# Optimization experiments

Measured on AMD Instinct MI355X. Metric: run time of the kernel, lower is better.

The kernel has to match this reference:

```python
import jax, jax.numpy as jnp
import numpy as np

N_NODES = 100000


def gcn_conv(x, edge_index, W, b, n_nodes):
    # h = X W  (transform first, aggregate in the smaller hidden dim)
    h = x @ W
    src, dst = edge_index[0], edge_index[1]
    # add self-loops (GCNConv default, fill_value=1)
    loop = jnp.arange(n_nodes, dtype=src.dtype)
    src = jnp.concatenate([src, loop])
    dst = jnp.concatenate([dst, loop])
    w = jnp.ones(src.shape[0], dtype=x.dtype)
    # symmetric degree normalization: deg^{-1/2}[src] * w * deg^{-1/2}[dst]
    deg = jax.ops.segment_sum(w, dst, num_segments=n_nodes)
    dinv = jnp.where(deg > 0, jax.lax.rsqrt(deg), 0.0).astype(x.dtype)
    norm = dinv[src] * w * dinv[dst]
    # gather messages from src, scale, scatter-add into dst
    out = jax.ops.segment_sum(h[src] * norm[:, None], dst, num_segments=n_nodes)
    return out + b


def setup_inputs() -> dict:
    key = jax.random.key(0)
    k1, k2, k3, k4 = jax.random.split(key, 4)
    n, f, hid, c, e = N_NODES, 512, 64, 40, 1600000
    x = jax.random.normal(k1, (n, f), dtype=jnp.float32)
    edge_index = jax.random.randint(k2, (2, e), 0, n, dtype=jnp.int64)
    W1 = jax.random.normal(k3, (f, hid), dtype=jnp.float32) * (1.0 / np.sqrt(f))
    b1 = jnp.zeros((hid,), dtype=jnp.float32)
    W2 = jax.random.normal(k4, (hid, c), dtype=jnp.float32) * (1.0 / np.sqrt(hid))
    b2 = jnp.zeros((c,), dtype=jnp.float32)
    return {"x": x, "edge_index": edge_index, "W1": W1, "b1": b1, "W2": W2, "b2": b2}


def reference(x, edge_index, W1, b1, W2, b2):
    h = jax.nn.relu(gcn_conv(x, edge_index, W1, b1, N_NODES))
    # dropout is identity at inference (training=False)
    h = gcn_conv(h, edge_index, W2, b2, N_NODES)
    return jax.nn.log_softmax(h, axis=1)
```

## Files before the change

kernel.cpp:

```cpp
#include <hip/hip_runtime.h>
#include <hip/hip_bf16.h>
#include <hip/hip_fp16.h>
#include <cstddef>

#define N_NODES 100000
#define F_IN    512
#define HID     64
#define NCLS    40

#define CAP       64
#define CUR_PAD   16

#define NPART       8
#define PART_NODES  12500
#define PART_BLOCKS 256

using half8 = __attribute__((ext_vector_type(8))) _Float16;
using f32x4 = __attribute__((ext_vector_type(4))) float;

__global__ void zero_kernel(int* __restrict__ p, int n) {
    int i = blockIdx.x * blockDim.x + threadIdx.x;
    if (i < n) p[i] = 0;
}

__global__ __launch_bounds__(256) void scatter_part_kernel(const int* __restrict__ src,
                                                           const int* __restrict__ dst,
                                                           int* __restrict__ cur,
                                                           int* __restrict__ ebuf, int E) {
    const int p  = blockIdx.x & (NPART - 1);
    const int bi = blockIdx.x >> 3;
    const int nb = gridDim.x >> 3;
    const int lo = p * PART_NODES, hi = lo + PART_NODES;
    for (int e = bi * 256 + (int)threadIdx.x; e < E; e += nb * 256) {
        int d = dst[e];
        if (d >= lo && d < hi) {
            int pos = atomicAdd(&cur[d * CUR_PAD], 1);
            if (pos < CAP) ebuf[(size_t)d * CAP + pos] = src[e];
        }
    }
}

__global__ void make_dinv_kernel(const int* __restrict__ cur, float* __restrict__ dinv, int n) {
    int i = blockIdx.x * blockDim.x + threadIdx.x;
    if (i < n) dinv[i] = rsqrtf((float)(cur[i * CUR_PAD] + 1));
}

__global__ __launch_bounds__(256) void gemm1_mfma_kernel(const float* __restrict__ X,
                                                         const float* __restrict__ W,
                                                         __half* __restrict__ H, int M) {
    __shared__ _Float16 As[4][64][8];
    __shared__ _Float16 Bs[4][64][8];

    const int tid  = threadIdx.x;
    const int lane = tid & 63;
    const int w    = tid >> 6;
    const int l15  = lane & 15;
    const int kg   = lane >> 4;
    const int rowBase = blockIdx.x * 64;

    f32x4 acc[4] = {};

    for (int kt = 0; kt < F_IN; kt += 32) {
        #pragma unroll
        for (int p = 0; p < 2; ++p) {
            int idx = tid * 2 + p;
            int r = idx >> 3, k4 = idx & 7;
            int gr = rowBase + r; if (gr >= M) gr = M - 1;
            const float4 v = *reinterpret_cast<const float4*>(
                &X[(size_t)gr * F_IN + kt + k4 * 4]);
            _Float16* dstp = &As[k4 >> 1][r][(k4 & 1) * 4];
            dstp[0] = (_Float16)v.x; dstp[1] = (_Float16)v.y;
            dstp[2] = (_Float16)v.z; dstp[3] = (_Float16)v.w;
        }
        #pragma unroll
        for (int p = 0; p < 2; ++p) {
            int idx = tid * 2 + p;
            int k = idx >> 4, c4 = idx & 15;
            const float4 v = *reinterpret_cast<const float4*>(
                &W[(size_t)(kt + k) * HID + c4 * 4]);
            int kgg = k >> 3, j = k & 7;
            Bs[kgg][c4 * 4 + 0][j] = (_Float16)v.x;
            Bs[kgg][c4 * 4 + 1][j] = (_Float16)v.y;
            Bs[kgg][c4 * 4 + 2][j] = (_Float16)v.z;
            Bs[kgg][c4 * 4 + 3][j] = (_Float16)v.w;
        }
        __syncthreads();

        const half8 a = *reinterpret_cast<const half8*>(&As[kg][w * 16 + l15][0]);
        #pragma unroll
        for (int ct = 0; ct < 4; ++ct) {
            const half8 b = *reinterpret_cast<const half8*>(&Bs[kg][ct * 16 + l15][0]);
            acc[ct] = __builtin_amdgcn_mfma_f32_16x16x32_f16(a, b, acc[ct], 0, 0, 0);
        }
        __syncthreads();
    }

    #pragma unroll
    for (int ct = 0; ct < 4; ++ct) {
        #pragma unroll
        for (int r = 0; r < 4; ++r) {
            int grow = rowBase + w * 16 + kg * 4 + r;
            if (grow < M) H[(size_t)grow * HID + ct * 16 + l15] = __float2half(acc[ct][r]);
        }
    }
}

__global__ __launch_bounds__(256) void agg1_kernel(const __half* __restrict__ h,
                                                   const int* __restrict__ ebuf,
                                                   const int* __restrict__ cur,
                                                   const float* __restrict__ dinv,
                                                   const float* __restrict__ b1,
                                                   __half* __restrict__ z, int M) {
    const int lane = threadIdx.x & 63;
    const int n = blockIdx.x * 4 + (threadIdx.x >> 6);
    if (n >= M) return;

    const float di = dinv[n];
    float acc = __half2float(h[(size_t)n * HID + lane]) * di * di;

    const int cnt = min(cur[n * CUR_PAD], CAP);
    const int* win = &ebuf[(size_t)n * CAP];

    int   s  = 0;
    float nm = 0.f;
    if (lane < cnt) {
        s  = win[lane];
        nm = dinv[s] * di;
    }
    int j = 0;
    for (; j + 4 <= cnt; j += 4) {
        int sa = __shfl(s, j);
        int sb = __shfl(s, j + 1);
        int sc = __shfl(s, j + 2);
        int sd = __shfl(s, j + 3);
        float na = __shfl(nm, j);
        float nb = __shfl(nm, j + 1);
        float nc = __shfl(nm, j + 2);
        float nd = __shfl(nm, j + 3);
        float va = __half2float(h[(size_t)sa * HID + lane]);
        float vb = __half2float(h[(size_t)sb * HID + lane]);
        float vc = __half2float(h[(size_t)sc * HID + lane]);
        float vd = __half2float(h[(size_t)sd * HID + lane]);
        acc = fmaf(va, na, acc);
        acc = fmaf(vb, nb, acc);
        acc = fmaf(vc, nc, acc);
        acc = fmaf(vd, nd, acc);
    }
    for (; j < cnt; ++j) {
        int sj = __shfl(s, j);
        float nj = __shfl(nm, j);
        acc = fmaf(__half2float(h[(size_t)sj * HID + lane]), nj, acc);
    }

    acc = fmaxf(acc + b1[lane], 0.0f);
    z[(size_t)n * HID + lane] = __float2half(acc);
}

__global__ __launch_bounds__(256) void gemm2_kernel(const __half* __restrict__ z,
                                                    const float* __restrict__ W2,
                                                    __half* __restrict__ h2, int M) {
    __shared__ float W2s[HID * NCLS];
    __shared__ float zs[64 * HID];

    const int tid = threadIdx.x;
    const int rowBase = blockIdx.x * 64;

    for (int i = tid; i < HID * NCLS; i += 256) W2s[i] = W2[i];

    #pragma unroll
    for (int p = 0; p < 2; ++p) {
        int o = tid * 2 + p;
        int r = o >> 3, c8 = o & 7;
        int gr = rowBase + r;
        float4 raw = make_float4(0.f, 0.f, 0.f, 0.f);
        if (gr < M) raw = *reinterpret_cast<const float4*>(&z[(size_t)gr * HID + c8 * 8]);
        const __half2* hp = reinterpret_cast<const __half2*>(&raw);
        #pragma unroll
        for (int q = 0; q < 4; ++q) {
            float2 f = __half22float2(hp[q]);
            zs[r * HID + c8 * 8 + q * 2]     = f.x;
            zs[r * HID + c8 * 8 + q * 2 + 1] = f.y;
        }
    }
    __syncthreads();

    #pragma unroll
    for (int p = 0; p < 10; ++p) {
        int o = p * 256 + tid;
        int r = o / NCLS, j = o - r * NCLS;
        float s = 0.f;
        #pragma unroll
        for (int k = 0; k < HID; ++k) s = fmaf(zs[r * HID + k], W2s[k * NCLS + j], s);
        int gr = rowBase + r;
        if (gr < M) h2[(size_t)gr * 64 + j] = __float2half(s);
    }
}

__global__ __launch_bounds__(256) void agg2_lsm_kernel(const __half* __restrict__ h2,
                                                       const int* __restrict__ ebuf,
                                                       const int* __restrict__ cur,
                                                       const float* __restrict__ dinv,
                                                       const float* __restrict__ b2,
                                                       float* __restrict__ out, int M) {
    const int lane = threadIdx.x & 63;
    const int n = blockIdx.x * 4 + (threadIdx.x >> 6);
    if (n >= M) return;

    const bool act = (lane < NCLS);
    const float di = dinv[n];
    float acc = act ? __half2float(h2[(size_t)n * 64 + lane]) * di * di : 0.f;

    const int cnt = min(cur[n * CUR_PAD], CAP);
    const int* win = &ebuf[(size_t)n * CAP];

    int   s  = 0;
    float nm = 0.f;
    if (lane < cnt) {
        s  = win[lane];
        nm = dinv[s] * di;
    }
    int j = 0;
    for (; j + 4 <= cnt; j += 4) {
        int sa = __shfl(s, j);
        int sb = __shfl(s, j + 1);
        int sc = __shfl(s, j + 2);
        int sd = __shfl(s, j + 3);
        float na = __shfl(nm, j);
        float nb = __shfl(nm, j + 1);
        float nc = __shfl(nm, j + 2);
        float nd = __shfl(nm, j + 3);
        if (act) {
            float va = __half2float(h2[(size_t)sa * 64 + lane]);
            float vb = __half2float(h2[(size_t)sb * 64 + lane]);
            float vc = __half2float(h2[(size_t)sc * 64 + lane]);
            float vd = __half2float(h2[(size_t)sd * 64 + lane]);
            acc = fmaf(va, na, acc);
            acc = fmaf(vb, nb, acc);
            acc = fmaf(vc, nc, acc);
            acc = fmaf(vd, nd, acc);
        }
    }
    for (; j < cnt; ++j) {
        int sj = __shfl(s, j);
        float nj = __shfl(nm, j);
        if (act) acc = fmaf(__half2float(h2[(size_t)sj * 64 + lane]), nj, acc);
    }

    float logit = act ? (acc + b2[lane]) : -1e30f;
    float m = logit;
    #pragma unroll
    for (int o = 32; o >= 1; o >>= 1) m = fmaxf(m, __shfl_xor(m, o));
    float ex = act ? __expf(logit - m) : 0.f;
    float sm = ex;
    #pragma unroll
    for (int o = 32; o >= 1; o >>= 1) sm += __shfl_xor(sm, o);
    float res = logit - m - __logf(sm);

    if (act) out[(size_t)n * NCLS + lane] = res;
}

extern "C" void kernel_launch(void* const* d_in, const int* in_sizes, int n_in,
                              void* d_out, int out_size, void* d_ws, size_t ws_size,
                              hipStream_t stream) {
    const float* x  = (const float*)d_in[0];
    const int*   ei = (const int*)d_in[1];
    const float* W1 = (const float*)d_in[2];
    const float* b1 = (const float*)d_in[3];
    const float* W2 = (const float*)d_in[4];
    const float* b2 = (const float*)d_in[5];
    float* out = (float*)d_out;

    const int M = N_NODES;
    const int E = in_sizes[1] / 2;
    const int* src = ei;
    const int* dst = ei + E;

    char* ws = (char*)d_ws;
    int*    cur  = (int*)   (ws + 0);
    float*  dinv = (float*) (ws + 6400000);
    int*    ebuf = (int*)   (ws + 6800000);
    __half* h1   = (__half*)(ws + 32400000);
    __half* z    = (__half*)(ws + 45200000);
    __half* h2   = (__half*)(ws + 58000000);

    zero_kernel<<<(M * CUR_PAD + 255) / 256, 256, 0, stream>>>(cur, M * CUR_PAD);

    scatter_part_kernel<<<NPART * PART_BLOCKS, 256, 0, stream>>>(src, dst, cur, ebuf, E);
    make_dinv_kernel<<<(M + 255) / 256, 256, 0, stream>>>(cur, dinv, M);

    gemm1_mfma_kernel<<<(M + 63) / 64, 256, 0, stream>>>(x, W1, h1, M);

    agg1_kernel<<<(M + 3) / 4, 256, 0, stream>>>(h1, ebuf, cur, dinv, b1, z, M);

    gemm2_kernel<<<(M + 63) / 64, 256, 0, stream>>>(z, W2, h2, M);
    agg2_lsm_kernel<<<(M + 3) / 4, 256, 0, stream>>>(h2, ebuf, cur, dinv, b2, out, M);
}
```

Before: 295.5 us.

## Fuse layer-1 aggregation with second GEMM and unpad degree counters

Merges the layer-1 aggregation kernel with the 64x40 second transform, so each block aggregates four nodes, keeps the ReLU outputs in shared memory and multiplies them by W2 directly. This removes the z intermediate buffer, one kernel launch, and the global-memory round trip for z. It also drops the 16-int padding on the per-node atomic counters, which shrinks the zeroing and counter traffic but may bring back contention from atomics that share a cache line. In exchange, every block reloads the whole W2 into shared memory and only 160 of 256 threads take part in the small GEMM.

```diff
diff --git a/kernel.cpp b/kernel.cpp
--- a/kernel.cpp
+++ b/kernel.cpp
@@ -9,7 +9,6 @@
 #define NCLS    40
 
 #define CAP       64
-#define CUR_PAD   16
 
 #define NPART       8
 #define PART_NODES  12500
@@ -34,7 +33,7 @@
     for (int e = bi * 256 + (int)threadIdx.x; e < E; e += nb * 256) {
         int d = dst[e];
         if (d >= lo && d < hi) {
-            int pos = atomicAdd(&cur[d * CUR_PAD], 1);
+            int pos = atomicAdd(&cur[d], 1);
             if (pos < CAP) ebuf[(size_t)d * CAP + pos] = src[e];
         }
     }
@@ -42,7 +41,7 @@
 
 __global__ void make_dinv_kernel(const int* __restrict__ cur, float* __restrict__ dinv, int n) {
     int i = blockIdx.x * blockDim.x + threadIdx.x;
-    if (i < n) dinv[i] = rsqrtf((float)(cur[i * CUR_PAD] + 1));
+    if (i < n) dinv[i] = rsqrtf((float)(cur[i] + 1));
 }
 
 __global__ __launch_bounds__(256) void gemm1_mfma_kernel(const float* __restrict__ X,
@@ -105,20 +104,27 @@
     }
 }
 
-__global__ __launch_bounds__(256) void agg1_kernel(const __half* __restrict__ h,
-                                                   const int* __restrict__ ebuf,
-                                                   const int* __restrict__ cur,
-                                                   const float* __restrict__ dinv,
-                                                   const float* __restrict__ b1,
-                                                   __half* __restrict__ z, int M) {
-    const int lane = threadIdx.x & 63;
-    const int n = blockIdx.x * 4 + (threadIdx.x >> 6);
-    if (n >= M) return;
+__global__ __launch_bounds__(256) void agg1_gemm2_kernel(const __half* __restrict__ h,
+                                                         const int* __restrict__ ebuf,
+                                                         const int* __restrict__ cur,
+                                                         const float* __restrict__ dinv,
+                                                         const float* __restrict__ b1,
+                                                         const float* __restrict__ W2,
+                                                         __half* __restrict__ h2) {
+    __shared__ float W2s[HID * NCLS];
+    __shared__ float zt[4][HID];
+
+    const int tid  = threadIdx.x;
+    const int lane = tid & 63;
+    const int wv   = tid >> 6;
+    const int n    = blockIdx.x * 4 + wv;
+
+    for (int i = tid; i < HID * NCLS; i += 256) W2s[i] = W2[i];
 
     const float di = dinv[n];
     float acc = __half2float(h[(size_t)n * HID + lane]) * di * di;
 
-    const int cnt = min(cur[n * CUR_PAD], CAP);
+    const int cnt = min(cur[n], CAP);
     const int* win = &ebuf[(size_t)n * CAP];
 
     int   s  = 0;
@@ -152,47 +158,16 @@
         acc = fmaf(__half2float(h[(size_t)sj * HID + lane]), nj, acc);
     }
 
-    acc = fmaxf(acc + b1[lane], 0.0f);
-    z[(size_t)n * HID + lane] = __float2half(acc);
-}
-
-__global__ __launch_bounds__(256) void gemm2_kernel(const __half* __restrict__ z,
-                                                    const float* __restrict__ W2,
-                                                    __half* __restrict__ h2, int M) {
-    __shared__ float W2s[HID * NCLS];
-    __shared__ float zs[64 * HID];
-
-    const int tid = threadIdx.x;
-    const int rowBase = blockIdx.x * 64;
-
-    for (int i = tid; i < HID * NCLS; i += 256) W2s[i] = W2[i];
-
-    #pragma unroll
-    for (int p = 0; p < 2; ++p) {
-        int o = tid * 2 + p;
-        int r = o >> 3, c8 = o & 7;
-        int gr = rowBase + r;
-        float4 raw = make_float4(0.f, 0.f, 0.f, 0.f);
-        if (gr < M) raw = *reinterpret_cast<const float4*>(&z[(size_t)gr * HID + c8 * 8]);
-        const __half2* hp = reinterpret_cast<const __half2*>(&raw);
-        #pragma unroll
-        for (int q = 0; q < 4; ++q) {
-            float2 f = __half22float2(hp[q]);
-            zs[r * HID + c8 * 8 + q * 2]     = f.x;
-            zs[r * HID + c8 * 8 + q * 2 + 1] = f.y;
-        }
-    }
+    zt[wv][lane] = fmaxf(acc + b1[lane], 0.0f);
     __syncthreads();
 
-    #pragma unroll
-    for (int p = 0; p < 10; ++p) {
-        int o = p * 256 + tid;
-        int r = o / NCLS, j = o - r * NCLS;
-        float s = 0.f;
-        #pragma unroll
-        for (int k = 0; k < HID; ++k) s = fmaf(zs[r * HID + k], W2s[k * NCLS + j], s);
-        int gr = rowBase + r;
-        if (gr < M) h2[(size_t)gr * 64 + j] = __float2half(s);
+    if (tid < 4 * NCLS) {
+        int r = tid / NCLS, c = tid - r * NCLS;
+        float sacc = 0.f;
+        #pragma unroll
+        for (int k = 0; k < HID; ++k)
+            sacc = fmaf(zt[r][k], W2s[k * NCLS + c], sacc);
+        h2[(size_t)(blockIdx.x * 4 + r) * 64 + c] = __float2half(sacc);
     }
 }
 
@@ -210,7 +185,7 @@
     const float di = dinv[n];
     float acc = act ? __half2float(h2[(size_t)n * 64 + lane]) * di * di : 0.f;
 
-    const int cnt = min(cur[n * CUR_PAD], CAP);
+    const int cnt = min(cur[n], CAP);
     const int* win = &ebuf[(size_t)n * CAP];
 
     int   s  = 0;
@@ -277,21 +252,19 @@
 
     char* ws = (char*)d_ws;
     int*    cur  = (int*)   (ws + 0);
-    float*  dinv = (float*) (ws + 6400000);
-    int*    ebuf = (int*)   (ws + 6800000);
-    __half* h1   = (__half*)(ws + 32400000);
-    __half* z    = (__half*)(ws + 45200000);
-    __half* h2   = (__half*)(ws + 58000000);
-
-    zero_kernel<<<(M * CUR_PAD + 255) / 256, 256, 0, stream>>>(cur, M * CUR_PAD);
+    float*  dinv = (float*) (ws + 409600);
+    int*    ebuf = (int*)   (ws + 819200);
+    __half* h1   = (__half*)(ws + 26419200);
+    __half* h2   = (__half*)(ws + 39219200);
+
+    zero_kernel<<<(M + 255) / 256, 256, 0, stream>>>(cur, M);
 
     scatter_part_kernel<<<NPART * PART_BLOCKS, 256, 0, stream>>>(src, dst, cur, ebuf, E);
     make_dinv_kernel<<<(M + 255) / 256, 256, 0, stream>>>(cur, dinv, M);
 
     gemm1_mfma_kernel<<<(M + 63) / 64, 256, 0, stream>>>(x, W1, h1, M);
 
-    agg1_kernel<<<(M + 3) / 4, 256, 0, stream>>>(h1, ebuf, cur, dinv, b1, z, M);
-
-    gemm2_kernel<<<(M + 63) / 64, 256, 0, stream>>>(z, W2, h2, M);
+    agg1_gemm2_kernel<<<M / 4, 256, 0, stream>>>(h1, ebuf, cur, dinv, b1, W2, h2);
+
     agg2_lsm_kernel<<<(M + 3) / 4, 256, 0, stream>>>(h2, ebuf, cur, dinv, b2, out, M);
 }
```

Result: no change. 294.8 us (-0.2%).
